# Kernel tuning notes

Hardware: AMD Instinct MI355X
Metric: run time of the kernel (lower is better)

The kernel has to match this reference:

```python
import jax, jax.numpy as jnp
import numpy as np

B, T, S, D, H, DH = 2, 2048, 2048, 1024, 16, 64
LN_EPS = 1e-5


def setup_inputs() -> dict:
    key = jax.random.key(0)
    ks = jax.random.split(key, 8)
    return {
        "x": jax.random.normal(ks[0], (B, T, D), jnp.float32),
        "context": jax.random.normal(ks[1], (B, S, D), jnp.float32),
        "lookup_table": jax.random.normal(ks[2], (2 * T - 1, DH), jnp.float32),
        "Wq": jax.random.normal(ks[3], (D, H * DH), jnp.float32) * 0.02,
        "Wk": jax.random.normal(ks[4], (D, H * DH), jnp.float32) * 0.02,
        "Wv": jax.random.normal(ks[5], (D, H * DH), jnp.float32) * 0.02,
        "Wo": jax.random.normal(ks[6], (H * DH, D), jnp.float32) * 0.02,
        "bo": jnp.zeros((D,), jnp.float32),
        "gamma": jnp.ones((D,), jnp.float32),
        "beta": jnp.zeros((D,), jnp.float32),
    }


def skew(QE):
    # QE: [B, H, T, 2T-1] -> [B, H, T, T] via pad/reshape relative-position trick
    b, h, t, _ = QE.shape
    QE = jnp.pad(QE, ((0, 0), (0, 0), (0, 0), (0, 1))).reshape(b, h, -1)
    QE = jnp.pad(QE, ((0, 0), (0, 0), (0, t - 1))).reshape(b, h, t + 1, 2 * t - 1)
    return QE[:, :, :t, -t:]


def reference(x, context, lookup_table, Wq, Wk, Wv, Wo, bo, gamma, beta):
    scale = 1.0 / jnp.sqrt(jnp.asarray(DH, x.dtype))
    # pre-layernorm on queries
    mu = jnp.mean(x, axis=-1, keepdims=True)
    var = jnp.var(x, axis=-1, keepdims=True)
    xn = (x - mu) / jnp.sqrt(var + LN_EPS) * gamma + beta
    q = (xn @ Wq).reshape(B, T, H, DH).transpose(0, 2, 1, 3)       # [B,H,T,DH]
    k = (context @ Wk).reshape(B, S, H, DH).transpose(0, 2, 1, 3)  # [B,H,S,DH]
    v = (context @ Wv).reshape(B, S, H, DH).transpose(0, 2, 1, 3)  # [B,H,S,DH]
    score = jnp.einsum("bhtd,bhsd->bhts", q, k) * scale            # [B,H,T,S]
    rel = skew(jnp.einsum("bhtd,ld->bhtl", q, lookup_table))       # [B,H,T,T]
    # NOTE: faithful to original — QK^T gets scaled twice, rel term once
    score = (score + rel) * scale
    attn = jax.nn.softmax(score, axis=-1)
    out = jnp.einsum("bhts,bhsd->bhtd", attn, v)
    out = out.transpose(0, 2, 1, 3).reshape(B, T, H * DH)
    out = out @ Wo + bo
    # dropout=0 (eval); residual uses the layernormed x (as in source)
    return xn + out
```

## Files before the change

### kernel.cpp

```cpp
#include <hip/hip_runtime.h>

#define DEVFN __device__ __forceinline__

typedef __bf16 bf16x8 __attribute__((ext_vector_type(8)));
typedef float f32x4 __attribute__((ext_vector_type(4)));
typedef unsigned short u16;


DEVFN u16 f2bf(float f) {
  unsigned u = __builtin_bit_cast(unsigned, f);
  u += 0x7FFFu + ((u >> 16) & 1u);
  return (u16)(u >> 16);
}

DEVFN f32x4 mfma16(bf16x8 a, bf16x8 b, f32x4 c) {
  return __builtin_amdgcn_mfma_f32_16x16x32_bf16(a, b, c, 0, 0, 0);
}

DEVFN void gl16(const u16* g, u16* l) {
  __builtin_amdgcn_global_load_lds(
      (const __attribute__((address_space(1))) unsigned int*)g,
      (__attribute__((address_space(3))) unsigned int*)l, 16, 0, 0);
}

__global__ __launch_bounds__(256) void ln_kernel(const float* __restrict__ x,
                                                 const float* __restrict__ gamma,
                                                 const float* __restrict__ beta,
                                                 float* __restrict__ xn,
                                                 u16* __restrict__ xnb) {
  int row = blockIdx.x;
  int tid = threadIdx.x;
  const float4* xr = (const float4*)(x + (size_t)row * 1024);
  float4 v = xr[tid];
  float s = v.x + v.y + v.z + v.w;
  float q = v.x * v.x + v.y * v.y + v.z * v.z + v.w * v.w;
#pragma unroll
  for (int m = 1; m < 64; m <<= 1) {
    s += __shfl_xor(s, m);
    q += __shfl_xor(q, m);
  }
  __shared__ float rs[4], rq[4];
  int w = tid >> 6;
  if ((tid & 63) == 0) { rs[w] = s; rq[w] = q; }
  __syncthreads();
  s = rs[0] + rs[1] + rs[2] + rs[3];
  q = rq[0] + rq[1] + rq[2] + rq[3];
  float mean = s * (1.0f / 1024.0f);
  float var = q * (1.0f / 1024.0f) - mean * mean;
  float inv = rsqrtf(var + 1e-5f);
  float4 g = ((const float4*)gamma)[tid];
  float4 bt = ((const float4*)beta)[tid];
  float4 o;
  o.x = (v.x - mean) * inv * g.x + bt.x;
  o.y = (v.y - mean) * inv * g.y + bt.y;
  o.z = (v.z - mean) * inv * g.z + bt.z;
  o.w = (v.w - mean) * inv * g.w + bt.w;
  ((float4*)(xn + (size_t)row * 1024))[tid] = o;
  ushort4 ob;
  ob.x = f2bf(o.x); ob.y = f2bf(o.y); ob.z = f2bf(o.z); ob.w = f2bf(o.w);
  ((ushort4*)(xnb + (size_t)row * 1024))[tid] = ob;
}

__global__ __launch_bounds__(256) void cvt_kernel(const float* __restrict__ in,
                                                  u16* __restrict__ out, int n4) {
  int i = blockIdx.x * 256 + threadIdx.x;
  if (i < n4) {
    float4 v = ((const float4*)in)[i];
    ushort4 o;
    o.x = f2bf(v.x); o.y = f2bf(v.y); o.z = f2bf(v.z); o.w = f2bf(v.w);
    ((ushort4*)out)[i] = o;
  }
}

__global__ __launch_bounds__(256) void transW_kernel(const float* __restrict__ W0,
                                                     const float* __restrict__ W1,
                                                     const float* __restrict__ W2,
                                                     const float* __restrict__ W3,
                                                     u16* __restrict__ Wall) {
  __shared__ float tile[32][33];
  int z = blockIdx.z;
  const float* W = (z == 0) ? W0 : (z == 1) ? W1 : (z == 2) ? W2 : W3;
  float scale = (z == 0) ? 0.18033688011112042f : (z == 1) ? 0.125f : 1.0f;
  u16* Wt = Wall + (size_t)z * 1048576;
  int tx = threadIdx.x, ty = threadIdx.y;
  int x = blockIdx.x * 32 + tx;
  int y0 = blockIdx.y * 32;
#pragma unroll
  for (int j = 0; j < 32; j += 8)
    tile[ty + j][tx] = W[(size_t)(y0 + ty + j) * 1024 + x];
  __syncthreads();
#pragma unroll
  for (int j = 0; j < 32; j += 8)
    Wt[(size_t)(blockIdx.x * 32 + ty + j) * 1024 + y0 + tx] = f2bf(tile[tx][ty + j] * scale);
}

DEVFN void gemm_core(const u16* __restrict__ A, const u16* __restrict__ Bt,
                     u16* Ab, u16* Bb, int row0, int n0, int tid,
                     f32x4 (&acc)[2][4]) {
  int lane = tid & 63, wv = tid >> 6;
  int l16 = lane & 15, lhi = lane >> 4;
  int r8 = lane >> 3, c8 = lane & 7;
  int cx = ((c8 ^ r8) << 3);
  int swz = (l16 & 7) << 3;

  auto stage = [&](int k0) {
#pragma unroll
    for (int i = 0; i < 4; ++i) {
      int rowb = wv * 32 + i * 8;
      gl16(&A[(size_t)(row0 + rowb + r8) * 1024 + k0 + cx], &Ab[rowb * 64]);
    }
#pragma unroll
    for (int i = 0; i < 2; ++i) {
      int rowb = wv * 16 + i * 8;
      gl16(&Bt[(size_t)(n0 + rowb + r8) * 1024 + k0 + cx], &Bb[rowb * 64]);
    }
  };

  stage(0);
  asm volatile("s_waitcnt vmcnt(0)" ::: "memory");
  __syncthreads();
  for (int kk = 0; kk < 16; ++kk) {
    __builtin_amdgcn_s_setprio(1);
#pragma unroll
    for (int ks = 0; ks < 2; ++ks) {
      bf16x8 af[2], bfr[4];
#pragma unroll
      for (int mi = 0; mi < 2; ++mi) {
        int row = wv * 32 + mi * 16 + l16;
        af[mi] = *(const bf16x8*)&Ab[row * 64 + ((ks * 32 + lhi * 8) ^ swz)];
      }
#pragma unroll
      for (int ni = 0; ni < 4; ++ni) {
        int row = ni * 16 + l16;
        bfr[ni] = *(const bf16x8*)&Bb[row * 64 + ((ks * 32 + lhi * 8) ^ swz)];
      }
#pragma unroll
      for (int mi = 0; mi < 2; ++mi)
#pragma unroll
        for (int ni = 0; ni < 4; ++ni)
          acc[mi][ni] = mfma16(af[mi], bfr[ni], acc[mi][ni]);
    }
    __builtin_amdgcn_s_setprio(0);
    if (kk < 15) {
      __syncthreads();
      stage((kk + 1) * 64);
      asm volatile("s_waitcnt vmcnt(0)" ::: "memory");
      __syncthreads();
    }
  }
}

__global__ __launch_bounds__(256, 4) void qkv_kernel(const u16* __restrict__ xnb,
                                                     const u16* __restrict__ ctxb,
                                                     const u16* __restrict__ Wall,
                                                     u16* __restrict__ qb,
                                                     u16* __restrict__ kb,
                                                     u16* __restrict__ vtb) {
  __shared__ __align__(16) u16 Ab[128 * 64];
  __shared__ __align__(16) u16 Bb[64 * 64];
  int z = blockIdx.z;
  const u16* A = (z == 0) ? xnb : ctxb;
  const u16* Bt = Wall + (size_t)z * 1048576;
  int row0 = blockIdx.x * 128, n0 = blockIdx.y * 64;
  f32x4 acc[2][4] = {};
  gemm_core(A, Bt, Ab, Bb, row0, n0, threadIdx.x, acc);
  int tid = threadIdx.x, lane = tid & 63, wv = tid >> 6;
  int l16 = lane & 15, lhi = lane >> 4;
  u16* qk = (z == 0) ? qb : kb;
#pragma unroll
  for (int mi = 0; mi < 2; ++mi)
#pragma unroll
    for (int ni = 0; ni < 4; ++ni)
#pragma unroll
      for (int r = 0; r < 4; ++r) {
        int m = row0 + wv * 32 + mi * 16 + lhi * 4 + r;
        int n = n0 + ni * 16 + l16;
        int b = m >> 11, t = m & 2047, h = n >> 6, dh = n & 63;
        u16 val = f2bf(acc[mi][ni][r]);
        if (z < 2)
          qk[(size_t)((b * 16 + h) * 2048 + t) * 64 + dh] = val;
        else
          vtb[(size_t)((b * 16 + h) * 64 + dh) * 2048 + t] = val;
      }
}

__global__ __launch_bounds__(256, 4) void oproj_kernel(const u16* __restrict__ attnb,
                                                       const u16* __restrict__ Wall,
                                                       const float* __restrict__ bias,
                                                       const float* __restrict__ resid,
                                                       float* __restrict__ outF) {
  __shared__ __align__(16) u16 Ab[128 * 64];
  __shared__ __align__(16) u16 Bb[64 * 64];
  const u16* Bt = Wall + (size_t)3 * 1048576;
  int row0 = blockIdx.x * 128, n0 = blockIdx.y * 64;
  f32x4 acc[2][4] = {};
  gemm_core(attnb, Bt, Ab, Bb, row0, n0, threadIdx.x, acc);
  int tid = threadIdx.x, lane = tid & 63, wv = tid >> 6;
  int l16 = lane & 15, lhi = lane >> 4;
#pragma unroll
  for (int mi = 0; mi < 2; ++mi)
#pragma unroll
    for (int ni = 0; ni < 4; ++ni)
#pragma unroll
      for (int r = 0; r < 4; ++r) {
        int m = row0 + wv * 32 + mi * 16 + lhi * 4 + r;
        int n = n0 + ni * 16 + l16;
        outF[(size_t)m * 1024 + n] = acc[mi][ni][r] + bias[n] + resid[(size_t)m * 1024 + n];
      }
}

__global__ __launch_bounds__(256, 4) void flash_kernel(
    const u16* __restrict__ Qg, const u16* __restrict__ Kg,
    const u16* __restrict__ Vtg, const u16* __restrict__ Lb,
    u16* __restrict__ Og) {
  constexpr int T = 2048, H = 16;
  int p = blockIdx.x;
  int bid = (p & 7) * 128 + (p >> 3);
  int qb = bid & 31, h = (bid >> 5) & 15, b = bid >> 9;
  int tid = threadIdx.x;
  int lane = tid & 63, w = tid >> 6;
  int l16 = lane & 15, lhi = lane >> 4;

  __shared__ __align__(16) u16 Klds[64 * 64];
  __shared__ __align__(16) u16 Vt[64 * 64];
  __shared__ __align__(16) u16 Plds[4][16 * 64];

  const u16* qbase = Qg + (size_t)(b * H + h) * T * 64;
  const u16* kbase = Kg + (size_t)(b * H + h) * T * 64;
  const u16* vtbase = Vtg + (size_t)(b * H + h) * 64 * 2048;

  int i0w = qb * 64 + w * 16;
  bf16x8 aq[2];
  aq[0] = *(const bf16x8*)&qbase[(i0w + l16) * 64 + lhi * 8];
  aq[1] = *(const bf16x8*)&qbase[(i0w + l16) * 64 + 32 + lhi * 8];

  f32x4 accO[4] = {};
  float mrun[4], lsum[4];
#pragma unroll
  for (int r = 0; r < 4; ++r) { mrun[r] = -1e30f; lsum[r] = 0.0f; }

  int bandbase = T - 16 - i0w;

  int r8 = lane >> 3, c8 = lane & 7;
  int cx = ((c8 ^ r8) << 3);
  int swz = (l16 & 7) << 3;

  auto stage = [&](int j0) {
#pragma unroll
    for (int i = 0; i < 2; ++i) {
      int rowb = w * 16 + i * 8;
      gl16(&kbase[(size_t)(j0 + rowb + r8) * 64 + cx], &Klds[rowb * 64]);
    }
#pragma unroll
    for (int i = 0; i < 2; ++i) {
      int rowb = w * 16 + i * 8;
      gl16(&vtbase[(size_t)(rowb + r8) * 2048 + j0 + cx], &Vt[rowb * 64]);
    }
  };

  f32x4 eC = {};
#pragma unroll
  for (int ks = 0; ks < 2; ++ks) {
    int u = bandbase + l16;
    u = min(max(u, 0), 2 * T - 2);
    bf16x8 bl = *(const bf16x8*)&Lb[(size_t)u * 64 + ks * 32 + lhi * 8];
    eC = mfma16(aq[ks], bl, eC);
  }

  const float THR = 11.541560327111707f;

  for (int kt = 0; kt < 32; ++kt) {
    int j0 = kt * 64, bstart = bandbase + j0;
    stage(j0);

    f32x4 accE[5];
    accE[0] = eC;
#pragma unroll
    for (int c = 1; c < 5; ++c) accE[c] = f32x4{0.f, 0.f, 0.f, 0.f};
#pragma unroll
    for (int ks = 0; ks < 2; ++ks) {
      bf16x8 bl[4];
#pragma unroll
      for (int c = 1; c < 5; ++c) {
        int u = bstart + c * 16 + l16;
        u = min(max(u, 0), 2 * T - 2);
        bl[c - 1] = *(const bf16x8*)&Lb[(size_t)u * 64 + ks * 32 + lhi * 8];
      }
#pragma unroll
      for (int c = 1; c < 5; ++c) accE[c] = mfma16(aq[ks], bl[c - 1], accE[c]);
    }
    eC = accE[4];

    __syncthreads();

    f32x4 accS[4] = {};
    __builtin_amdgcn_s_setprio(1);
#pragma unroll
    for (int ks = 0; ks < 2; ++ks)
#pragma unroll
      for (int kb = 0; kb < 4; ++kb) {
        int row = kb * 16 + l16;
        bf16x8 bk = *(const bf16x8*)&Klds[row * 64 + ((ks * 32 + lhi * 8) ^ swz)];
        accS[kb] = mfma16(aq[ks], bk, accS[kb]);
      }
    __builtin_amdgcn_s_setprio(0);

    float sc[4][4];
    float lm[4];
    bool need = false;
#pragma unroll
    for (int r = 0; r < 4; ++r) {
      int m = lhi * 4 + r;
      int srcl = lhi * 16 + ((l16 - m + 15) & 15);
      bool lo = (l16 <= m);
      float e[5];
#pragma unroll
      for (int c = 0; c < 5; ++c) e[c] = __shfl(accE[c][r], srcl);
#pragma unroll
      for (int kb = 0; kb < 4; ++kb) sc[r][kb] = accS[kb][r] + (lo ? e[kb] : e[kb + 1]);
      lm[r] = fmaxf(fmaxf(sc[r][0], sc[r][1]), fmaxf(sc[r][2], sc[r][3]));
      need |= (lm[r] > mrun[r] + THR);
    }
    if (__ballot(need)) {
#pragma unroll
      for (int r = 0; r < 4; ++r) {
        float tm = lm[r];
        tm = fmaxf(tm, __shfl_xor(tm, 1));
        tm = fmaxf(tm, __shfl_xor(tm, 2));
        tm = fmaxf(tm, __shfl_xor(tm, 4));
        tm = fmaxf(tm, __shfl_xor(tm, 8));
        float mnew = fmaxf(mrun[r], tm);
        float al = exp2f(mrun[r] - mnew);
        mrun[r] = mnew;
        lsum[r] *= al;
#pragma unroll
        for (int dt = 0; dt < 4; ++dt) accO[dt][r] *= al;
      }
    }
#pragma unroll
    for (int r = 0; r < 4; ++r) {
      int m = lhi * 4 + r;
      int swm = (m & 7) << 3;
      float mm = mrun[r], ps = 0.0f;
#pragma unroll
      for (int kb = 0; kb < 4; ++kb) {
        float pv = exp2f(sc[r][kb] - mm);
        ps += pv;
        Plds[w][m * 64 + ((kb * 16 + l16) ^ swm)] = f2bf(pv);
      }
      lsum[r] += ps;
    }

    __builtin_amdgcn_s_setprio(1);
#pragma unroll
    for (int ks = 0; ks < 2; ++ks) {
      bf16x8 ap = *(const bf16x8*)&Plds[w][l16 * 64 + ((ks * 32 + lhi * 8) ^ ((l16 & 7) << 3))];
#pragma unroll
      for (int dt = 0; dt < 4; ++dt) {
        int row = dt * 16 + l16;
        bf16x8 bv = *(const bf16x8*)&Vt[row * 64 + ((ks * 32 + lhi * 8) ^ swz)];
        accO[dt] = mfma16(ap, bv, accO[dt]);
      }
    }
    __builtin_amdgcn_s_setprio(0);
    __syncthreads();
  }

#pragma unroll
  for (int r = 0; r < 4; ++r) {
    float l = lsum[r];
    l += __shfl_xor(l, 1);
    l += __shfl_xor(l, 2);
    l += __shfl_xor(l, 4);
    l += __shfl_xor(l, 8);
    lsum[r] = 1.0f / l;
  }
#pragma unroll
  for (int dt = 0; dt < 4; ++dt)
#pragma unroll
    for (int r = 0; r < 4; ++r) {
      int i = i0w + lhi * 4 + r;
      int col = h * 64 + dt * 16 + l16;
      Og[(size_t)(b * T + i) * 1024 + col] = f2bf(accO[dt][r] * lsum[r]);
    }
}

extern "C" void kernel_launch(void* const* d_in, const int* in_sizes, int n_in,
                              void* d_out, int out_size, void* d_ws, size_t ws_size,
                              hipStream_t stream) {
  const float* x = (const float*)d_in[0];
  const float* ctx = (const float*)d_in[1];
  const float* Ltab = (const float*)d_in[2];
  const float* Wq = (const float*)d_in[3];
  const float* Wk = (const float*)d_in[4];
  const float* Wv = (const float*)d_in[5];
  const float* Wo = (const float*)d_in[6];
  const float* bo = (const float*)d_in[7];
  const float* gamma = (const float*)d_in[8];
  const float* beta = (const float*)d_in[9];
  float* out = (float*)d_out;

  size_t off = 0;
  auto take = [&](size_t bytes) {
    void* p = (char*)d_ws + off;
    off += (bytes + 255) & ~(size_t)255;
    return p;
  };
  u16* xnb = (u16*)take(8388608);
  u16* ctxb = (u16*)take(8388608);
  u16* Lb = (u16*)take(4095 * 64 * 2);
  u16* Wall = (u16*)take(4 * 2097152);
  u16* qbuf = (u16*)take(8388608);
  u16* kbuf = (u16*)take(8388608);
  u16* vtbuf = (u16*)take(8388608);
  u16* attnb = (u16*)take(8388608);

  ln_kernel<<<dim3(4096), dim3(256), 0, stream>>>(x, gamma, beta, out, xnb);
  cvt_kernel<<<dim3(4096), dim3(256), 0, stream>>>(ctx, ctxb, 1048576);
  cvt_kernel<<<dim3(256), dim3(256), 0, stream>>>(Ltab, Lb, 65520);
  transW_kernel<<<dim3(32, 32, 4), dim3(32, 8), 0, stream>>>(Wq, Wk, Wv, Wo, Wall);
  qkv_kernel<<<dim3(32, 16, 3), dim3(256), 0, stream>>>(xnb, ctxb, Wall, qbuf, kbuf, vtbuf);
  flash_kernel<<<dim3(1024), dim3(256), 0, stream>>>(qbuf, kbuf, vtbuf, Lb, attnb);
  oproj_kernel<<<dim3(32, 16), dim3(256), 0, stream>>>(attnb, Wall, bo, out, out);
}
```

Measured before the change: 229.3 us.

## Split flash attention over key halves and merge partials in a combine kernel

Each query tile's 32 key tiles are split across two blocks. Each block writes unnormalized partial outputs in bf16 plus running max and sum to a workspace, and a new combine kernel merges the two halves with log-sum-exp rescaling. The goal is to double the block count (1024 to 2048) and raise occupancy (launch bounds 4 to 6) so the 256 CUs stay busier. The cost is an extra kernel launch, extra global traffic for the partials, and one more bf16 rounding of the partial outputs. The xn bf16 buffer is reused as the partial buffer after the QKV projection.

```diff
diff --git a/kernel.cpp b/kernel.cpp
--- a/kernel.cpp
+++ b/kernel.cpp
@@ -11,6 +11,10 @@
   unsigned u = __builtin_bit_cast(unsigned, f);
   u += 0x7FFFu + ((u >> 16) & 1u);
   return (u16)(u >> 16);
+}
+
+DEVFN float bf2f(u16 v) {
+  return __builtin_bit_cast(float, (unsigned)v << 16);
 }
 
 DEVFN f32x4 mfma16(bf16x8 a, bf16x8 b, f32x4 c) {
@@ -209,14 +213,17 @@
       }
 }
 
-__global__ __launch_bounds__(256, 4) void flash_kernel(
+__global__ __launch_bounds__(256, 6) void flash_kernel(
     const u16* __restrict__ Qg, const u16* __restrict__ Kg,
     const u16* __restrict__ Vtg, const u16* __restrict__ Lb,
-    u16* __restrict__ Og) {
+    u16* __restrict__ pbuf, float* __restrict__ mlb) {
   constexpr int T = 2048, H = 16;
   int p = blockIdx.x;
-  int bid = (p & 7) * 128 + (p >> 3);
-  int qb = bid & 31, h = (bid >> 5) & 15, b = bid >> 9;
+  int bid = (p & 7) * 256 + (p >> 3);
+  int half = bid & 1;
+  int cid = bid >> 1;
+  int qb = cid & 31, h = (cid >> 5) & 15, b = cid >> 9;
+  int st = half * 16;
   int tid = threadIdx.x;
   int lane = tid & 63, w = tid >> 6;
   int l16 = lane & 15, lhi = lane >> 4;
@@ -261,7 +268,7 @@
   f32x4 eC = {};
 #pragma unroll
   for (int ks = 0; ks < 2; ++ks) {
-    int u = bandbase + l16;
+    int u = bandbase + st * 64 + l16;
     u = min(max(u, 0), 2 * T - 2);
     bf16x8 bl = *(const bf16x8*)&Lb[(size_t)u * 64 + ks * 32 + lhi * 8];
     eC = mfma16(aq[ks], bl, eC);
@@ -269,7 +276,7 @@
 
   const float THR = 11.541560327111707f;
 
-  for (int kt = 0; kt < 32; ++kt) {
+  for (int kt = st; kt < st + 16; ++kt) {
     int j0 = kt * 64, bstart = bandbase + j0;
     stage(j0);
 
@@ -366,6 +373,7 @@
     __syncthreads();
   }
 
+  int pidx = cid * 2 + half;
 #pragma unroll
   for (int r = 0; r < 4; ++r) {
     float l = lsum[r];
@@ -373,16 +381,58 @@
     l += __shfl_xor(l, 2);
     l += __shfl_xor(l, 4);
     l += __shfl_xor(l, 8);
-    lsum[r] = 1.0f / l;
-  }
-#pragma unroll
-  for (int dt = 0; dt < 4; ++dt)
-#pragma unroll
-    for (int r = 0; r < 4; ++r) {
-      int i = i0w + lhi * 4 + r;
-      int col = h * 64 + dt * 16 + l16;
-      Og[(size_t)(b * T + i) * 1024 + col] = f2bf(accO[dt][r] * lsum[r]);
-    }
+    lsum[r] = l;
+  }
+#pragma unroll
+  for (int r = 0; r < 4; ++r) {
+    int row = w * 16 + lhi * 4 + r;
+    if (l16 == 0) {
+      mlb[((size_t)pidx * 64 + row) * 2] = mrun[r];
+      mlb[((size_t)pidx * 64 + row) * 2 + 1] = lsum[r];
+    }
+#pragma unroll
+    for (int dt = 0; dt < 4; ++dt)
+      pbuf[((size_t)pidx * 64 + row) * 64 + dt * 16 + l16] = f2bf(accO[dt][r]);
+  }
+}
+
+__global__ __launch_bounds__(256) void combine_kernel(const u16* __restrict__ pbuf,
+                                                      const float* __restrict__ mlb,
+                                                      u16* __restrict__ attnb) {
+  int cid = blockIdx.x;
+  int qb = cid & 31, h = (cid >> 5) & 15, b = cid >> 9;
+  int tid = threadIdx.x;
+  int row = tid >> 2, qd = (tid & 3) * 16;
+  size_t base0 = ((size_t)(cid * 2) * 64 + row) * 64 + qd;
+  size_t base1 = base0 + 4096;
+  const float* m0 = mlb + ((size_t)(cid * 2) * 64 + row) * 2;
+  float m1 = m0[0], l1 = m0[1], m2 = m0[128], l2 = m0[129];
+  float mm = fmaxf(m1, m2);
+  float a1 = exp2f(m1 - mm), a2 = exp2f(m2 - mm);
+  float inv = 1.0f / (a1 * l1 + a2 * l2);
+  a1 *= inv;
+  a2 *= inv;
+  uint4 x[2], y[2];
+  x[0] = *(const uint4*)&pbuf[base0];
+  x[1] = *(const uint4*)&pbuf[base0 + 8];
+  y[0] = *(const uint4*)&pbuf[base1];
+  y[1] = *(const uint4*)&pbuf[base1 + 8];
+  uint4 o[2];
+#pragma unroll
+  for (int v = 0; v < 2; ++v) {
+    unsigned* xu = (unsigned*)&x[v];
+    unsigned* yu = (unsigned*)&y[v];
+    unsigned* ou = (unsigned*)&o[v];
+#pragma unroll
+    for (int j = 0; j < 4; ++j) {
+      float f0 = bf2f((u16)(xu[j] & 0xffff)), f1 = bf2f((u16)(xu[j] >> 16));
+      float g0 = bf2f((u16)(yu[j] & 0xffff)), g1 = bf2f((u16)(yu[j] >> 16));
+      ou[j] = (unsigned)f2bf(f0 * a1 + g0 * a2) | ((unsigned)f2bf(f1 * a1 + g1 * a2) << 16);
+    }
+  }
+  size_t dst = ((size_t)(b * 2048 + qb * 64 + row)) * 1024 + h * 64 + qd;
+  *(uint4*)&attnb[dst] = o[0];
+  *(uint4*)&attnb[dst + 8] = o[1];
 }
 
 extern "C" void kernel_launch(void* const* d_in, const int* in_sizes, int n_in,
@@ -414,12 +464,15 @@
   u16* kbuf = (u16*)take(8388608);
   u16* vtbuf = (u16*)take(8388608);
   u16* attnb = (u16*)take(8388608);
+  float* mlb = (float*)take(2048 * 64 * 2 * 4);
+  u16* pbuf = xnb;
 
   ln_kernel<<<dim3(4096), dim3(256), 0, stream>>>(x, gamma, beta, out, xnb);
   cvt_kernel<<<dim3(4096), dim3(256), 0, stream>>>(ctx, ctxb, 1048576);
   cvt_kernel<<<dim3(256), dim3(256), 0, stream>>>(Ltab, Lb, 65520);
   transW_kernel<<<dim3(32, 32, 4), dim3(32, 8), 0, stream>>>(Wq, Wk, Wv, Wo, Wall);
   qkv_kernel<<<dim3(32, 16, 3), dim3(256), 0, stream>>>(xnb, ctxb, Wall, qbuf, kbuf, vtbuf);
-  flash_kernel<<<dim3(1024), dim3(256), 0, stream>>>(qbuf, kbuf, vtbuf, Lb, attnb);
+  flash_kernel<<<dim3(2048), dim3(256), 0, stream>>>(qbuf, kbuf, vtbuf, Lb, pbuf, mlb);
+  combine_kernel<<<dim3(1024), dim3(256), 0, stream>>>(pbuf, mlb, attnb);
   oproj_kernel<<<dim3(32, 16), dim3(256), 0, stream>>>(attnb, Wall, bo, out, out);
 }
```

Measured after the change: 414.5 us. 80.8% more time.

## Load K/V fragments directly from global into registers, dropping LDS staging and barriers

Applied to the files above, without the earlier changes.

The flash attention loop no longer stages K and V tiles into LDS with global_load_lds and block-wide __syncthreads. Each wave now reads its MFMA B-operand fragments for K and V straight from global memory into registers. It reuses one register array, prefetching the next K tile at the end of each iteration and loading V after the QK MFMAs. The lookup-table index clamping is removed and the rel-position MFMAs get raised priority. This trades the barriers and LDS traffic for four-fold redundant global/L2 reads across the waves of a block and more exposed load latency. The unclamped lookup reads can also run one row past the table end.

```diff
diff --git a/kernel.cpp b/kernel.cpp
--- a/kernel.cpp
+++ b/kernel.cpp
@@ -221,8 +221,6 @@
   int lane = tid & 63, w = tid >> 6;
   int l16 = lane & 15, lhi = lane >> 4;
 
-  __shared__ __align__(16) u16 Klds[64 * 64];
-  __shared__ __align__(16) u16 Vt[64 * 64];
   __shared__ __align__(16) u16 Plds[4][16 * 64];
 
   const u16* qbase = Qg + (size_t)(b * H + h) * T * 64;
@@ -240,70 +238,63 @@
   for (int r = 0; r < 4; ++r) { mrun[r] = -1e30f; lsum[r] = 0.0f; }
 
   int bandbase = T - 16 - i0w;
-
-  int r8 = lane >> 3, c8 = lane & 7;
-  int cx = ((c8 ^ r8) << 3);
+  const u16* kp = kbase + l16 * 64 + lhi * 8;
+  const u16* vp = vtbase + l16 * 2048 + lhi * 8;
+  const u16* lp = Lb + (size_t)(bandbase + l16) * 64 + lhi * 8;
+
+  f32x4 eC = {};
+#pragma unroll
+  for (int ks = 0; ks < 2; ++ks)
+    eC = mfma16(aq[ks], *(const bf16x8*)&lp[ks * 32], eC);
+
+  bf16x8 fr[8];
+#pragma unroll
+  for (int ks = 0; ks < 2; ++ks)
+#pragma unroll
+    for (int kb = 0; kb < 4; ++kb)
+      fr[ks * 4 + kb] = *(const bf16x8*)&kp[kb * 1024 + ks * 32];
+
+  const float THR = 11.541560327111707f;
   int swz = (l16 & 7) << 3;
 
-  auto stage = [&](int j0) {
-#pragma unroll
-    for (int i = 0; i < 2; ++i) {
-      int rowb = w * 16 + i * 8;
-      gl16(&kbase[(size_t)(j0 + rowb + r8) * 64 + cx], &Klds[rowb * 64]);
-    }
-#pragma unroll
-    for (int i = 0; i < 2; ++i) {
-      int rowb = w * 16 + i * 8;
-      gl16(&vtbase[(size_t)(rowb + r8) * 2048 + j0 + cx], &Vt[rowb * 64]);
-    }
-  };
-
-  f32x4 eC = {};
-#pragma unroll
-  for (int ks = 0; ks < 2; ++ks) {
-    int u = bandbase + l16;
-    u = min(max(u, 0), 2 * T - 2);
-    bf16x8 bl = *(const bf16x8*)&Lb[(size_t)u * 64 + ks * 32 + lhi * 8];
-    eC = mfma16(aq[ks], bl, eC);
-  }
-
-  const float THR = 11.541560327111707f;
-
   for (int kt = 0; kt < 32; ++kt) {
-    int j0 = kt * 64, bstart = bandbase + j0;
-    stage(j0);
+    const u16* lpt = lp + kt * 4096;
+    const u16* vpt = vp + kt * 64;
+
+    bf16x8 bl[8];
+#pragma unroll
+    for (int ks = 0; ks < 2; ++ks)
+#pragma unroll
+      for (int c = 1; c < 5; ++c)
+        bl[ks * 4 + c - 1] = *(const bf16x8*)&lpt[c * 1024 + ks * 32];
+
+    f32x4 accS[4] = {};
+    __builtin_amdgcn_s_setprio(1);
+#pragma unroll
+    for (int ks = 0; ks < 2; ++ks)
+#pragma unroll
+      for (int kb = 0; kb < 4; ++kb)
+        accS[kb] = mfma16(aq[ks], fr[ks * 4 + kb], accS[kb]);
+    __builtin_amdgcn_s_setprio(0);
+
+#pragma unroll
+    for (int ks = 0; ks < 2; ++ks)
+#pragma unroll
+      for (int dt = 0; dt < 4; ++dt)
+        fr[ks * 4 + dt] = *(const bf16x8*)&vpt[dt * 32768 + ks * 32];
 
     f32x4 accE[5];
     accE[0] = eC;
 #pragma unroll
     for (int c = 1; c < 5; ++c) accE[c] = f32x4{0.f, 0.f, 0.f, 0.f};
-#pragma unroll
-    for (int ks = 0; ks < 2; ++ks) {
-      bf16x8 bl[4];
-#pragma unroll
-      for (int c = 1; c < 5; ++c) {
-        int u = bstart + c * 16 + l16;
-        u = min(max(u, 0), 2 * T - 2);
-        bl[c - 1] = *(const bf16x8*)&Lb[(size_t)u * 64 + ks * 32 + lhi * 8];
-      }
-#pragma unroll
-      for (int c = 1; c < 5; ++c) accE[c] = mfma16(aq[ks], bl[c - 1], accE[c]);
-    }
+    __builtin_amdgcn_s_setprio(1);
+#pragma unroll
+    for (int ks = 0; ks < 2; ++ks)
+#pragma unroll
+      for (int c = 1; c < 5; ++c)
+        accE[c] = mfma16(aq[ks], bl[ks * 4 + c - 1], accE[c]);
+    __builtin_amdgcn_s_setprio(0);
     eC = accE[4];
-
-    __syncthreads();
-
-    f32x4 accS[4] = {};
-    __builtin_amdgcn_s_setprio(1);
-#pragma unroll
-    for (int ks = 0; ks < 2; ++ks)
-#pragma unroll
-      for (int kb = 0; kb < 4; ++kb) {
-        int row = kb * 16 + l16;
-        bf16x8 bk = *(const bf16x8*)&Klds[row * 64 + ((ks * 32 + lhi * 8) ^ swz)];
-        accS[kb] = mfma16(aq[ks], bk, accS[kb]);
-      }
-    __builtin_amdgcn_s_setprio(0);
 
     float sc[4][4];
     float lm[4];
@@ -354,16 +345,21 @@
     __builtin_amdgcn_s_setprio(1);
 #pragma unroll
     for (int ks = 0; ks < 2; ++ks) {
-      bf16x8 ap = *(const bf16x8*)&Plds[w][l16 * 64 + ((ks * 32 + lhi * 8) ^ ((l16 & 7) << 3))];
-#pragma unroll
-      for (int dt = 0; dt < 4; ++dt) {
-        int row = dt * 16 + l16;
-        bf16x8 bv = *(const bf16x8*)&Vt[row * 64 + ((ks * 32 + lhi * 8) ^ swz)];
-        accO[dt] = mfma16(ap, bv, accO[dt]);
-      }
+      bf16x8 ap = *(const bf16x8*)&Plds[w][l16 * 64 + ((ks * 32 + lhi * 8) ^ swz)];
+#pragma unroll
+      for (int dt = 0; dt < 4; ++dt)
+        accO[dt] = mfma16(ap, fr[ks * 4 + dt], accO[dt]);
     }
     __builtin_amdgcn_s_setprio(0);
-    __syncthreads();
+
+    if (kt < 31) {
+      const u16* kpt = kp + (kt + 1) * 4096;
+#pragma unroll
+      for (int ks = 0; ks < 2; ++ks)
+#pragma unroll
+        for (int kb = 0; kb < 4; ++kb)
+          fr[ks * 4 + kb] = *(const bf16x8*)&kpt[kb * 1024 + ks * 32];
+    }
   }
 
 #pragma unroll
```

After: 445.8 us. 94.4% more time.

## Split flash attention along key dimension into three parts with combine kernel

Applied to the files above, without the earlier changes.

Splits each query block's 32 key tiles across three workgroups (split-K flash decoding style), launching 3072 blocks instead of 1024. Each part writes its unnormalized bf16 partial output plus running max and sum, and a new combine kernel rescales and merges the partials into the attention buffer. This raises the number of blocks to better fill the GPU's compute units, at the cost of extra global writes and reads of partials, an extra kernel launch, and reuse of the xn bf16 buffer as scratch.

```diff
diff --git a/kernel.cpp b/kernel.cpp
--- a/kernel.cpp
+++ b/kernel.cpp
@@ -11,6 +11,10 @@
   unsigned u = __builtin_bit_cast(unsigned, f);
   u += 0x7FFFu + ((u >> 16) & 1u);
   return (u16)(u >> 16);
+}
+
+DEVFN float bf2f(u16 v) {
+  return __builtin_bit_cast(float, (unsigned)v << 16);
 }
 
 DEVFN f32x4 mfma16(bf16x8 a, bf16x8 b, f32x4 c) {
@@ -212,11 +216,15 @@
 __global__ __launch_bounds__(256, 4) void flash_kernel(
     const u16* __restrict__ Qg, const u16* __restrict__ Kg,
     const u16* __restrict__ Vtg, const u16* __restrict__ Lb,
-    u16* __restrict__ Og) {
+    u16* __restrict__ pbuf01, u16* __restrict__ pbuf2, float* __restrict__ mlb) {
   constexpr int T = 2048, H = 16;
   int p = blockIdx.x;
-  int bid = (p & 7) * 128 + (p >> 3);
-  int qb = bid & 31, h = (bid >> 5) & 15, b = bid >> 9;
+  int bid = (p & 7) * 384 + (p >> 3);
+  int cid = bid / 3;
+  int part = bid - cid * 3;
+  int qb = cid & 31, h = (cid >> 5) & 15, b = cid >> 9;
+  int st = part * 11;
+  int en = (part == 2) ? 32 : st + 11;
   int tid = threadIdx.x;
   int lane = tid & 63, w = tid >> 6;
   int l16 = lane & 15, lhi = lane >> 4;
@@ -261,7 +269,7 @@
   f32x4 eC = {};
 #pragma unroll
   for (int ks = 0; ks < 2; ++ks) {
-    int u = bandbase + l16;
+    int u = bandbase + st * 64 + l16;
     u = min(max(u, 0), 2 * T - 2);
     bf16x8 bl = *(const bf16x8*)&Lb[(size_t)u * 64 + ks * 32 + lhi * 8];
     eC = mfma16(aq[ks], bl, eC);
@@ -269,7 +277,7 @@
 
   const float THR = 11.541560327111707f;
 
-  for (int kt = 0; kt < 32; ++kt) {
+  for (int kt = st; kt < en; ++kt) {
     int j0 = kt * 64, bstart = bandbase + j0;
     stage(j0);
 
@@ -354,7 +362,7 @@
     __builtin_amdgcn_s_setprio(1);
 #pragma unroll
     for (int ks = 0; ks < 2; ++ks) {
-      bf16x8 ap = *(const bf16x8*)&Plds[w][l16 * 64 + ((ks * 32 + lhi * 8) ^ ((l16 & 7) << 3))];
+      bf16x8 ap = *(const bf16x8*)&Plds[w][l16 * 64 + ((ks * 32 + lhi * 8) ^ swz)];
 #pragma unroll
       for (int dt = 0; dt < 4; ++dt) {
         int row = dt * 16 + l16;
@@ -366,6 +374,9 @@
     __syncthreads();
   }
 
+  u16* myp = ((part == 2) ? pbuf2 : pbuf01 + (size_t)part * 4194304) +
+             (size_t)cid * 4096;
+  float* myml = mlb + ((size_t)(part * 1024 + cid) * 64) * 2;
 #pragma unroll
   for (int r = 0; r < 4; ++r) {
     float l = lsum[r];
@@ -373,16 +384,78 @@
     l += __shfl_xor(l, 2);
     l += __shfl_xor(l, 4);
     l += __shfl_xor(l, 8);
-    lsum[r] = 1.0f / l;
-  }
-#pragma unroll
-  for (int dt = 0; dt < 4; ++dt)
-#pragma unroll
-    for (int r = 0; r < 4; ++r) {
-      int i = i0w + lhi * 4 + r;
-      int col = h * 64 + dt * 16 + l16;
-      Og[(size_t)(b * T + i) * 1024 + col] = f2bf(accO[dt][r] * lsum[r]);
-    }
+    lsum[r] = l;
+  }
+#pragma unroll
+  for (int r = 0; r < 4; ++r) {
+    int row = w * 16 + lhi * 4 + r;
+    if (l16 == 0) {
+      myml[row * 2] = mrun[r];
+      myml[row * 2 + 1] = lsum[r];
+    }
+#pragma unroll
+    for (int dt = 0; dt < 4; ++dt)
+      myp[(size_t)row * 64 + dt * 16 + l16] = f2bf(accO[dt][r]);
+  }
+}
+
+__global__ __launch_bounds__(256) void combine_kernel(const u16* __restrict__ pbuf01,
+                                                      const u16* __restrict__ pbuf2,
+                                                      const float* __restrict__ mlb,
+                                                      u16* __restrict__ attnb) {
+  int cid = blockIdx.x;
+  int qb = cid & 31, h = (cid >> 5) & 15, b = cid >> 9;
+  int tid = threadIdx.x;
+  int row = tid >> 2, qd = (tid & 3) * 16;
+  float m[3], l[3];
+#pragma unroll
+  for (int p = 0; p < 3; ++p) {
+    const float* ml = mlb + ((size_t)(p * 1024 + cid) * 64 + row) * 2;
+    m[p] = ml[0];
+    l[p] = ml[1];
+  }
+  float mm = fmaxf(fmaxf(m[0], m[1]), m[2]);
+  float a[3];
+  float den = 0.0f;
+#pragma unroll
+  for (int p = 0; p < 3; ++p) {
+    a[p] = exp2f(m[p] - mm);
+    den += a[p] * l[p];
+  }
+  float inv = 1.0f / den;
+#pragma unroll
+  for (int p = 0; p < 3; ++p) a[p] *= inv;
+
+  float acc[16];
+#pragma unroll
+  for (int j = 0; j < 16; ++j) acc[j] = 0.0f;
+#pragma unroll
+  for (int p = 0; p < 3; ++p) {
+    const u16* src = ((p == 2) ? pbuf2 : pbuf01 + (size_t)p * 4194304) +
+                     (size_t)cid * 4096 + (size_t)row * 64 + qd;
+    uint4 x0 = *(const uint4*)&src[0];
+    uint4 x1 = *(const uint4*)&src[8];
+    const unsigned* xu = (const unsigned*)&x0;
+#pragma unroll
+    for (int j = 0; j < 4; ++j) {
+      acc[2 * j] += bf2f((u16)(xu[j] & 0xffff)) * a[p];
+      acc[2 * j + 1] += bf2f((u16)(xu[j] >> 16)) * a[p];
+    }
+    const unsigned* yu = (const unsigned*)&x1;
+#pragma unroll
+    for (int j = 0; j < 4; ++j) {
+      acc[8 + 2 * j] += bf2f((u16)(yu[j] & 0xffff)) * a[p];
+      acc[8 + 2 * j + 1] += bf2f((u16)(yu[j] >> 16)) * a[p];
+    }
+  }
+  uint4 o[2];
+  unsigned* ou = (unsigned*)&o[0];
+#pragma unroll
+  for (int j = 0; j < 8; ++j)
+    ou[j] = (unsigned)f2bf(acc[2 * j]) | ((unsigned)f2bf(acc[2 * j + 1]) << 16);
+  size_t dst = ((size_t)(b * 2048 + qb * 64 + row)) * 1024 + h * 64 + qd;
+  *(uint4*)&attnb[dst] = o[0];
+  *(uint4*)&attnb[dst + 8] = o[1];
 }
 
 extern "C" void kernel_launch(void* const* d_in, const int* in_sizes, int n_in,
@@ -414,12 +487,16 @@
   u16* kbuf = (u16*)take(8388608);
   u16* vtbuf = (u16*)take(8388608);
   u16* attnb = (u16*)take(8388608);
+  u16* pbuf2 = (u16*)take(8388608);
+  float* mlb = (float*)take(3 * 1024 * 64 * 2 * 4);
+  u16* pbuf01 = xnb;
 
   ln_kernel<<<dim3(4096), dim3(256), 0, stream>>>(x, gamma, beta, out, xnb);
   cvt_kernel<<<dim3(4096), dim3(256), 0, stream>>>(ctx, ctxb, 1048576);
   cvt_kernel<<<dim3(256), dim3(256), 0, stream>>>(Ltab, Lb, 65520);
   transW_kernel<<<dim3(32, 32, 4), dim3(32, 8), 0, stream>>>(Wq, Wk, Wv, Wo, Wall);
   qkv_kernel<<<dim3(32, 16, 3), dim3(256), 0, stream>>>(xnb, ctxb, Wall, qbuf, kbuf, vtbuf);
-  flash_kernel<<<dim3(1024), dim3(256), 0, stream>>>(qbuf, kbuf, vtbuf, Lb, attnb);
+  flash_kernel<<<dim3(3072), dim3(256), 0, stream>>>(qbuf, kbuf, vtbuf, Lb, pbuf01, pbuf2, mlb);
+  combine_kernel<<<dim3(1024), dim3(256), 0, stream>>>(pbuf01, pbuf2, mlb, attnb);
   oproj_kernel<<<dim3(32, 16), dim3(256), 0, stream>>>(attnb, Wall, bo, out, out);
 }
```

New measurement: 238.9 us. +4.2%, slower.
